# Optimization experiments

Measured on AMD Instinct MI355X. Metric: run time of the kernel, lower is better.

The kernel has to match this reference:

```python
import jax, jax.numpy as jnp
import numpy as np

N_USERS, N_ITEMS, N_TOPICS = 200000, 100000, 100
N_NODES = N_USERS + N_ITEMS + N_TOPICS
N_EDGES = 5000000
DIM = 64
LAYERS = 3
BATCH = 16384


def setup_inputs() -> dict:
    key = jax.random.key(0)
    ks = jax.random.split(key, 8)
    users = jax.random.randint(ks[0], (BATCH,), 0, N_USERS, dtype=jnp.int64 if jax.config.jax_enable_x64 else jnp.int32)
    items = jax.random.randint(ks[1], (BATCH,), 0, N_ITEMS, dtype=jnp.int64 if jax.config.jax_enable_x64 else jnp.int32)
    edge_rows = jax.random.randint(ks[2], (N_EDGES,), 0, N_NODES, dtype=jnp.int32)
    edge_cols = jax.random.randint(ks[3], (N_EDGES,), 0, N_NODES, dtype=jnp.int32)
    # values ~ 1/deg to mimic the symmetric-normalized A_hat of LightGCN
    edge_vals = jax.random.uniform(ks[4], (N_EDGES,), dtype=jnp.float32) / 16.0
    user_emb = 0.1 * jax.random.normal(ks[5], (N_USERS, DIM), dtype=jnp.float32)
    item_emb = 0.1 * jax.random.normal(ks[6], (N_ITEMS, DIM), dtype=jnp.float32)
    topic_emb = 0.1 * jax.random.normal(ks[7], (N_TOPICS, DIM), dtype=jnp.float32)
    return {"users": users, "items": items, "edge_rows": edge_rows,
            "edge_cols": edge_cols, "edge_vals": edge_vals,
            "user_emb": user_emb, "item_emb": item_emb, "topic_emb": topic_emb}


def reference(users, items, edge_rows, edge_cols, edge_vals, user_emb, item_emb, topic_emb):
    n_users = user_emb.shape[0]
    n_nodes = n_users + item_emb.shape[0] + topic_emb.shape[0]
    # E^0 = [users; items; topics]
    h = jnp.concatenate([user_emb, item_emb, topic_emb], axis=0)  # [N, dim]
    acc = h
    for _ in range(LAYERS):
        # sparse A_hat @ h : gather source rows, scale by edge weight, scatter-add to dst
        msgs = edge_vals[:, None] * h[edge_cols]                  # [E, dim]
        h = jax.ops.segment_sum(msgs, edge_rows, num_segments=n_nodes)
        acc = acc + h
    out = acc / (LAYERS + 1)                                      # stack-mean over layers
    u = out[users]                                                # [B, dim]
    it = out[n_users + items]                                     # items offset into node table
    return jnp.sum(u * it, axis=1)                                # [B]
```

## Files before the change

kernel.cpp:

```cpp
#include <hip/hip_runtime.h>
#include <hip/hip_fp16.h>

#define N_USERS  200000
#define N_ITEMS  100000
#define N_TOPICS 100
#define N_NODES  (N_USERS + N_ITEMS + N_TOPICS)
#define DIM      64
#define BSHIFT   10
#define BROWS    (1 << BSHIFT)
#define NBUCKETS ((N_NODES + BROWS - 1) >> BSHIFT)
#define NROWS_PAD (NBUCKETS * BROWS)
#define COLMASK  0x7FFFF
#define NB       512
#define NBSHIFT  9
#define M_TOT    (NBUCKETS * NB)
#define SB       256
#define CH       ((M_TOT + SB - 1) / SB)
#define NCONCAT  (((N_NODES * DIM / 4) + 511) / 512)
#define BUCKET_CAP 24576



__global__ void prep_kernel(const int* __restrict__ rows,
                            int* __restrict__ partial, int n_edges,
                            const float* __restrict__ uemb,
                            const float* __restrict__ iemb,
                            const float* __restrict__ temb,
                            ushort* __restrict__ h0,
                            const int* __restrict__ users,
                            const int* __restrict__ items,
                            float* __restrict__ u_acc,
                            float* __restrict__ it_acc, int B) {
    __shared__ int h[NBUCKETS];
    if (blockIdx.x < NB) {
        for (int i = threadIdx.x; i < NBUCKETS; i += blockDim.x) h[i] = 0;
        __syncthreads();
        int stride = NB * blockDim.x;
        int gid0 = blockIdx.x * blockDim.x + threadIdx.x;
        int n4 = n_edges >> 2;
        const int4* r4 = (const int4*)rows;
        for (int e = gid0; e < n4; e += stride) {
            int4 v = r4[e];
            atomicAdd(&h[((unsigned)v.x) >> BSHIFT], 1);
            atomicAdd(&h[((unsigned)v.y) >> BSHIFT], 1);
            atomicAdd(&h[((unsigned)v.z) >> BSHIFT], 1);
            atomicAdd(&h[((unsigned)v.w) >> BSHIFT], 1);
        }
        for (int e = (n4 << 2) + gid0; e < n_edges; e += stride)
            atomicAdd(&h[((unsigned)rows[e]) >> BSHIFT], 1);
        __syncthreads();
        for (int i = threadIdx.x; i < NBUCKETS; i += blockDim.x)
            partial[blockIdx.x * NBUCKETS + i] = h[i];
    } else if (blockIdx.x < NB + NCONCAT) {
        int g = (blockIdx.x - NB) * blockDim.x + threadIdx.x;
        long base = (long)g * 4;
        if (base >= (long)N_NODES * DIM) return;
        const float* src;
        long off;
        if (base < (long)N_USERS * DIM)                 { src = uemb; off = base; }
        else if (base < (long)(N_USERS + N_ITEMS) * DIM){ src = iemb; off = base - (long)N_USERS * DIM; }
        else                                            { src = temb; off = base - (long)(N_USERS + N_ITEMS) * DIM; }
        float4 v = *(const float4*)(src + off);
        __half2 a = __floats2half2_rn(v.x, v.y);
        __half2 b = __floats2half2_rn(v.z, v.w);
        uint2 o;
        o.x = *(unsigned*)&a;
        o.y = *(unsigned*)&b;
        ((uint2*)h0)[g] = o;
    } else {
        int g = (blockIdx.x - NB - NCONCAT) * blockDim.x + threadIdx.x;
        int b    = g >> 4;
        int lane = g & 15;
        if (b >= B) return;
        int u  = users[b];
        int it = items[b];
        float4 uv = ((const float4*)(uemb + (size_t)u  * DIM))[lane];
        float4 iv = ((const float4*)(iemb + (size_t)it * DIM))[lane];
        ((float4*)(u_acc  + (size_t)b * DIM))[lane] = uv;
        ((float4*)(it_acc + (size_t)b * DIM))[lane] = iv;
    }
}

__device__ __forceinline__ int phys_idx(int L) {
    return (L & (NB - 1)) * NBUCKETS + (L >> NBSHIFT);
}

__global__ void scanB1_kernel(const int* __restrict__ partial,
                              int* __restrict__ psum) {
    __shared__ int s[256];
    int tid = threadIdx.x;
    int c0 = blockIdx.x * CH;
    int c1 = min(M_TOT, c0 + CH);
    int sum = 0;
    for (int L = c0 + tid; L < c1; L += 256) sum += partial[phys_idx(L)];
    s[tid] = sum;
    __syncthreads();
    for (int off = 128; off > 0; off >>= 1) {
        if (tid < off) s[tid] += s[tid + off];
        __syncthreads();
    }
    if (tid == 0) psum[blockIdx.x] = s[0];
}

__global__ void scanB3_kernel(const int* __restrict__ partial,
                              const int* __restrict__ psum,
                              int* __restrict__ offs) {
    __shared__ int s[SB];
    __shared__ int tile[256];
    __shared__ int carry;
    int tid = threadIdx.x;
    s[tid] = (tid < blockIdx.x) ? psum[tid] : 0;
    __syncthreads();
    for (int off = 128; off > 0; off >>= 1) {
        if (tid < off) s[tid] += s[tid + off];
        __syncthreads();
    }
    if (tid == 0) carry = s[0];
    __syncthreads();
    int c0 = blockIdx.x * CH;
    int c1 = min(M_TOT, c0 + CH);
    for (int base = c0; base < c1; base += 256) {
        int L = base + tid;
        int v = (L < c1) ? partial[phys_idx(L)] : 0;
        tile[tid] = v;
        __syncthreads();
        for (int off = 1; off < 256; off <<= 1) {
            int t = (tid >= off) ? tile[tid - off] : 0;
            __syncthreads();
            tile[tid] += t;
            __syncthreads();
        }
        if (L < c1) offs[L] = carry + tile[tid] - v;
        __syncthreads();
        if (tid == 255) carry += tile[255];
        __syncthreads();
    }
}

__global__ void scatter1_kernel(const int* __restrict__ rows,
                                const int* __restrict__ cols,
                                const float* __restrict__ vals,
                                const int* __restrict__ offs,
                                int2* __restrict__ bkt_buf, int n_edges) {
    __shared__ int lpos[NBUCKETS];
    for (int i = threadIdx.x; i < NBUCKETS; i += blockDim.x)
        lpos[i] = offs[i * NB + blockIdx.x];
    __syncthreads();
    int stride = NB * blockDim.x;
    int gid0 = blockIdx.x * blockDim.x + threadIdx.x;
    int n4 = n_edges >> 2;
    const int4*   r4 = (const int4*)rows;
    const int4*   c4 = (const int4*)cols;
    const float4* v4 = (const float4*)vals;
    for (int e = gid0; e < n4; e += stride) {
        int4 r = r4[e];
        int4 c = c4[e];
        float4 v = v4[e];
        #pragma unroll
        for (int j = 0; j < 4; ++j) {
            int rr = (j == 0) ? r.x : (j == 1) ? r.y : (j == 2) ? r.z : r.w;
            int cc = (j == 0) ? c.x : (j == 1) ? c.y : (j == 2) ? c.z : c.w;
            float vv = (j == 0) ? v.x : (j == 1) ? v.y : (j == 2) ? v.z : v.w;
            int b = ((unsigned)rr) >> BSHIFT;
            int pos = atomicAdd(&lpos[b], 1);
            int2 p;
            p.x = cc | ((rr & (BROWS - 1)) << 19);
            p.y = __float_as_int(vv);
            bkt_buf[pos] = p;
        }
    }
    for (int e = (n4 << 2) + gid0; e < n_edges; e += stride) {
        int rr = rows[e];
        int b = ((unsigned)rr) >> BSHIFT;
        int pos = atomicAdd(&lpos[b], 1);
        int2 p;
        p.x = cols[e] | ((rr & (BROWS - 1)) << 19);
        p.y = __float_as_int(vals[e]);
        bkt_buf[pos] = p;
    }
}

__device__ __forceinline__ int pad8(int x) { return (x + 7) & ~7; }

__global__ void scatter2_kernel(const int2* __restrict__ bkt_buf,
                                const int* __restrict__ offs,
                                int2* __restrict__ row_span,
                                int2* __restrict__ csr_cv, int n_edges) {
    __shared__ int lcnt[BROWS];
    __shared__ int lptr[BROWS];
    __shared__ int lfill[BROWS];
    __shared__ int s[512];
    int b = blockIdx.x;
    int t = threadIdx.x;
    int e0 = offs[b * NB];
    int e1 = (b == NBUCKETS - 1) ? n_edges : offs[(b + 1) * NB];
    lcnt[t]  = 0;
    lfill[t] = 0;
    __syncthreads();
    for (int e = e0 + t; e < e1; e += 1024)
        atomicAdd(&lcnt[((unsigned)bkt_buf[e].x) >> 19], 1);
    __syncthreads();
    if (t < 512) s[t] = pad8(lcnt[2 * t]) + pad8(lcnt[2 * t + 1]);
    __syncthreads();
    for (int off = 1; off < 512; off <<= 1) {
        int v = 0;
        if (t < 512 && t >= off) v = s[t - off];
        __syncthreads();
        if (t < 512) s[t] += v;
        __syncthreads();
    }
    if (t < 512) {
        int base = b * BUCKET_CAP + (t ? s[t - 1] : 0);
        int rbase = b << BSHIFT;
        int pe = pad8(lcnt[2 * t]);
        int po = pad8(lcnt[2 * t + 1]);
        int p_even = base;
        int p_odd  = base + pe;
        lptr[2 * t]     = p_even;
        lptr[2 * t + 1] = p_odd;
        int2 sp0; sp0.x = p_even; sp0.y = p_even + pe;
        int2 sp1; sp1.x = p_odd;  sp1.y = p_odd + po;
        row_span[rbase + 2 * t]     = sp0;
        row_span[rbase + 2 * t + 1] = sp1;
    }
    __syncthreads();
    for (int e = e0 + t; e < e1; e += 1024) {
        int2 p = bkt_buf[e];
        int delta = ((unsigned)p.x) >> 19;
        int pos = lptr[delta] + atomicAdd(&lfill[delta], 1);
        int2 cv;
        cv.x = p.x & COLMASK;
        cv.y = p.y;
        csr_cv[pos] = cv;
    }
    __syncthreads();
    {
        int c  = lcnt[t];
        int cp = pad8(c);
        int p  = lptr[t];
        int2 z; z.x = 0; z.y = 0;
        for (int k = c; k < cp; ++k) csr_cv[p + k] = z;
    }
}

__device__ __forceinline__ float4 fma_mix4(const ushort* __restrict__ h,
                                           int row, int l16, float w,
                                           float4 acc) {
    uint2 r = ((const uint2*)(h + (size_t)row * DIM))[l16];
    __half2 h01 = *(__half2*)&r.x;
    __half2 h23 = *(__half2*)&r.y;
    acc.x = __builtin_fmaf(__half2float(__low2half(h01)),  w, acc.x);
    acc.y = __builtin_fmaf(__half2float(__high2half(h01)), w, acc.y);
    acc.z = __builtin_fmaf(__half2float(__low2half(h23)),  w, acc.z);
    acc.w = __builtin_fmaf(__half2float(__high2half(h23)), w, acc.w);
    return acc;
}

__device__ __forceinline__ float4 batch8(const int2* __restrict__ csr_cv,
                                         const ushort* __restrict__ h_src,
                                         int p, int l16, float4 acc) {
    const int4* q = (const int4*)(csr_cv + p);
    int4 a = q[0], b = q[1], c = q[2], d = q[3];
    acc = fma_mix4(h_src, a.x, l16, __int_as_float(a.y), acc);
    acc = fma_mix4(h_src, a.z, l16, __int_as_float(a.w), acc);
    acc = fma_mix4(h_src, b.x, l16, __int_as_float(b.y), acc);
    acc = fma_mix4(h_src, b.z, l16, __int_as_float(b.w), acc);
    acc = fma_mix4(h_src, c.x, l16, __int_as_float(c.y), acc);
    acc = fma_mix4(h_src, c.z, l16, __int_as_float(c.w), acc);
    acc = fma_mix4(h_src, d.x, l16, __int_as_float(d.y), acc);
    acc = fma_mix4(h_src, d.z, l16, __int_as_float(d.w), acc);
    return acc;
}

#define NWAVES ((N_NODES + 3) / 4)

__global__ void spmv_csr_kernel(const int2* __restrict__ row_span,
                                const int2* __restrict__ csr_cv,
                                const ushort* __restrict__ h_src,
                                ushort* __restrict__ h_dst,
                                const int* __restrict__ users,
                                const int* __restrict__ items,
                                float* __restrict__ u_acc,
                                float* __restrict__ it_acc,
                                int B, int first) {
    int wave = (int)(((long)blockIdx.x * blockDim.x + threadIdx.x) >> 6);
    int lane = threadIdx.x & 63;
    int g    = lane >> 4;
    int l16  = lane & 15;
    if (wave < NWAVES) {
        int r    = wave * 4 + g;
        int rc   = min(r, N_NODES - 1);
        int2 sp  = row_span[rc];
        int p0   = sp.x;
        int len  = (r < N_NODES) ? (sp.y - sp.x) : 0;
        int m = max(len, __shfl_xor(len, 16, 64));
        m = max(m, __shfl_xor(m, 32, 64));
        float4 acc = make_float4(0.f, 0.f, 0.f, 0.f);
        for (int off = 0; off < m; off += 8) {
            if (off < len)
                acc = batch8(csr_cv, h_src, p0 + off, l16, acc);
        }
        if (r < N_NODES) {
            __half2 a = __floats2half2_rn(acc.x, acc.y);
            __half2 b = __floats2half2_rn(acc.z, acc.w);
            uint2 o;
            o.x = *(unsigned*)&a;
            o.y = *(unsigned*)&b;
            ((uint2*)(h_dst + (size_t)r * DIM))[l16] = o;
        }
    } else {
        if (first < 0) return;
        int s = (wave - NWAVES) * 4 + g;
        if (s >= 2 * B) return;
        int node = (s < B) ? users[s] : (N_USERS + items[s - B]);
        uint2 hr = ((const uint2*)(h_src + (size_t)node * DIM))[l16];
        float2 a01 = __half22float2(*(__half2*)&hr.x);
        float2 a23 = __half22float2(*(__half2*)&hr.y);
        float* dst = (s < B) ? (u_acc + (size_t)s * DIM)
                             : (it_acc + (size_t)(s - B) * DIM);
        float4* p = (float4*)dst + l16;
        float4 o = *p;
        o.x += a01.x; o.y += a01.y; o.z += a23.x; o.w += a23.y;
        *p = o;
    }
}

__global__ void spmv_batch_dot_kernel(const int2* __restrict__ row_span,
                                      const int2* __restrict__ csr_cv,
                                      const ushort* __restrict__ h_src,
                                      const int* __restrict__ users,
                                      const int* __restrict__ items,
                                      const float* __restrict__ u_acc,
                                      const float* __restrict__ it_acc,
                                      float* __restrict__ out, int B) {
    int wave = (int)(((long)blockIdx.x * blockDim.x + threadIdx.x) >> 6);
    int lane = threadIdx.x & 63;
    int g    = lane >> 4;
    int l16  = lane & 15;
    int b    = wave * 2 + (g >> 1);
    bool ok  = b < B;
    int node = 0;
    if (ok) node = ((g & 1) == 0) ? users[b] : (N_USERS + items[b]);
    float4 acc = make_float4(0.f, 0.f, 0.f, 0.f);
    if (ok) {
        uint2 hr = ((const uint2*)(h_src + (size_t)node * DIM))[l16];
        float2 a01 = __half22float2(*(__half2*)&hr.x);
        float2 a23 = __half22float2(*(__half2*)&hr.y);
        acc = make_float4(a01.x, a01.y, a23.x, a23.y);
    }
    int2 sp  = row_span[ok ? node : 0];
    int p0   = sp.x;
    int len  = ok ? (sp.y - sp.x) : 0;
    int m = max(len, __shfl_xor(len, 16, 64));
    m = max(m, __shfl_xor(m, 32, 64));
    for (int off = 0; off < m; off += 8) {
        if (off < len)
            acc = batch8(csr_cv, h_src, p0 + off, l16, acc);
    }
    if (ok) {
        const float* st = ((g & 1) == 0) ? (u_acc  + (size_t)b * DIM)
                                         : (it_acc + (size_t)b * DIM);
        float4 sv = ((const float4*)st)[l16];
        acc.x += sv.x; acc.y += sv.y; acc.z += sv.z; acc.w += sv.w;
    }
    float px = __shfl_xor(acc.x, 16, 64);
    float py = __shfl_xor(acc.y, 16, 64);
    float pz = __shfl_xor(acc.z, 16, 64);
    float pw = __shfl_xor(acc.w, 16, 64);
    float p = acc.x * px + acc.y * py + acc.z * pz + acc.w * pw;
    p += __shfl_down(p, 8, 16);
    p += __shfl_down(p, 4, 16);
    p += __shfl_down(p, 2, 16);
    p += __shfl_down(p, 1, 16);
    if (ok && (g & 1) == 0 && l16 == 0) out[b] = p * (1.0f / 16.0f);
}

extern "C" void kernel_launch(void* const* d_in, const int* in_sizes, int n_in,
                              void* d_out, int out_size, void* d_ws, size_t ws_size,
                              hipStream_t stream) {
    const int*   users = (const int*)d_in[0];
    const int*   items = (const int*)d_in[1];
    const int*   erows = (const int*)d_in[2];
    const int*   ecols = (const int*)d_in[3];
    const float* evals = (const float*)d_in[4];
    const float* uemb  = (const float*)d_in[5];
    const float* iemb  = (const float*)d_in[6];
    const float* temb  = (const float*)d_in[7];
    float* out = (float*)d_out;

    const int n_edges = in_sizes[2];
    const int B       = in_sizes[0];

    const size_t h2bytes = (((size_t)N_NODES * DIM * 2 + 255) / 256) * 256;
    const size_t abytes  = (size_t)B * DIM * sizeof(float);
    const size_t spbytes = (((size_t)NROWS_PAD * 8 + 255) / 256) * 256;
    const size_t csrbytes= (size_t)NBUCKETS * BUCKET_CAP * 8;
    const size_t bkbytes = (size_t)n_edges * 8;
    const size_t mbytes  = (((size_t)M_TOT * 4 + 255) / 256) * 256;

    char* ws = (char*)d_ws;
    size_t off = 0;
    ushort* hA       = (ushort*)(ws + off); off += h2bytes;
    ushort* hB       = (ushort*)(ws + off); off += h2bytes;
    float*  u_acc    = (float*) (ws + off); off += abytes;
    float*  it_acc   = (float*) (ws + off); off += abytes;
    int2*   row_span = (int2*)  (ws + off); off += spbytes;
    int2*   csr_cv   = (int2*)  (ws + off); off += csrbytes;
    int2*   bkt_buf  = (int2*)  (ws + off); off += bkbytes;
    int*    partial  = (int*)   (ws + off); off += mbytes;
    int*    offs     = (int*)   (ws + off); off += mbytes;
    int*    psum     = (int*)   (ws + off); off += 4096;

    dim3 blk(256);
    dim3 blk512(512);
    dim3 blk1k(1024);

    const int ginit = (B * 16 + 511) / 512;
    prep_kernel<<<NB + NCONCAT + ginit, blk512, 0, stream>>>(
        erows, partial, n_edges, uemb, iemb, temb, hA,
        users, items, u_acc, it_acc, B);
    scanB1_kernel<<<SB, blk, 0, stream>>>(partial, psum);
    scanB3_kernel<<<SB, blk, 0, stream>>>(partial, psum, offs);
    scatter1_kernel<<<NB, blk512, 0, stream>>>(erows, ecols, evals, offs, bkt_buf, n_edges);
    scatter2_kernel<<<NBUCKETS, blk1k, 0, stream>>>(bkt_buf, offs, row_span,
                                                    csr_cv, n_edges);

    const int gwaves  = (2 * B + 3) / 4;
    const int blocks1 = (int)(((long)NWAVES * 64 + 255) / 256);
    const int blocks2 = (int)(((long)(NWAVES + gwaves) * 64 + 255) / 256);
    spmv_csr_kernel<<<blocks1, blk, 0, stream>>>(row_span, csr_cv, hA, hB,
                                                 users, items, u_acc, it_acc, B, -1);
    spmv_csr_kernel<<<blocks2, blk, 0, stream>>>(row_span, csr_cv, hB, hA,
                                                 users, items, u_acc, it_acc, B, 0);
    const int bwaves  = (B + 1) / 2;
    const int bblocks = (int)(((long)bwaves * 64 + 255) / 256);
    spmv_batch_dot_kernel<<<bblocks, blk, 0, stream>>>(row_span, csr_cv, hA,
                                                       users, items, u_acc, it_acc,
                                                       out, B);
}
```

Measured before the change: 502.6 us.

## Fuse the three SpMV layer kernels into one persistent cooperative kernel

Replaces the three separate launches (two SpMV layers and the final SpMV plus batch dot) with a single cooperative persistent kernel. Waves stride over the work, and grid-wide syncs separate the layers. This removes two kernel launch and drain gaps. In exchange, it caps concurrency at the occupancy limit and adds grid.sync overhead. The grid size assumes 256 CUs, which matches MI355X.

```diff
diff --git a/kernel.cpp b/kernel.cpp
--- a/kernel.cpp
+++ b/kernel.cpp
@@ -1,5 +1,8 @@
 #include <hip/hip_runtime.h>
 #include <hip/hip_fp16.h>
+#include <hip/hip_cooperative_groups.h>
+
+namespace cg = cooperative_groups;
 
 #define N_USERS  200000
 #define N_ITEMS  100000
@@ -274,71 +277,67 @@
 
 #define NWAVES ((N_NODES + 3) / 4)
 
-__global__ void spmv_csr_kernel(const int2* __restrict__ row_span,
-                                const int2* __restrict__ csr_cv,
-                                const ushort* __restrict__ h_src,
-                                ushort* __restrict__ h_dst,
-                                const int* __restrict__ users,
-                                const int* __restrict__ items,
-                                float* __restrict__ u_acc,
-                                float* __restrict__ it_acc,
-                                int B, int first) {
-    int wave = (int)(((long)blockIdx.x * blockDim.x + threadIdx.x) >> 6);
-    int lane = threadIdx.x & 63;
-    int g    = lane >> 4;
-    int l16  = lane & 15;
-    if (wave < NWAVES) {
-        int r    = wave * 4 + g;
-        int rc   = min(r, N_NODES - 1);
-        int2 sp  = row_span[rc];
-        int p0   = sp.x;
-        int len  = (r < N_NODES) ? (sp.y - sp.x) : 0;
-        int m = max(len, __shfl_xor(len, 16, 64));
-        m = max(m, __shfl_xor(m, 32, 64));
-        float4 acc = make_float4(0.f, 0.f, 0.f, 0.f);
-        for (int off = 0; off < m; off += 8) {
-            if (off < len)
-                acc = batch8(csr_cv, h_src, p0 + off, l16, acc);
-        }
-        if (r < N_NODES) {
-            __half2 a = __floats2half2_rn(acc.x, acc.y);
-            __half2 b = __floats2half2_rn(acc.z, acc.w);
-            uint2 o;
-            o.x = *(unsigned*)&a;
-            o.y = *(unsigned*)&b;
-            ((uint2*)(h_dst + (size_t)r * DIM))[l16] = o;
-        }
-    } else {
-        if (first < 0) return;
-        int s = (wave - NWAVES) * 4 + g;
-        if (s >= 2 * B) return;
-        int node = (s < B) ? users[s] : (N_USERS + items[s - B]);
-        uint2 hr = ((const uint2*)(h_src + (size_t)node * DIM))[l16];
-        float2 a01 = __half22float2(*(__half2*)&hr.x);
-        float2 a23 = __half22float2(*(__half2*)&hr.y);
-        float* dst = (s < B) ? (u_acc + (size_t)s * DIM)
-                             : (it_acc + (size_t)(s - B) * DIM);
-        float4* p = (float4*)dst + l16;
-        float4 o = *p;
-        o.x += a01.x; o.y += a01.y; o.z += a23.x; o.w += a23.y;
-        *p = o;
-    }
-}
-
-__global__ void spmv_batch_dot_kernel(const int2* __restrict__ row_span,
-                                      const int2* __restrict__ csr_cv,
-                                      const ushort* __restrict__ h_src,
-                                      const int* __restrict__ users,
-                                      const int* __restrict__ items,
-                                      const float* __restrict__ u_acc,
-                                      const float* __restrict__ it_acc,
-                                      float* __restrict__ out, int B) {
-    int wave = (int)(((long)blockIdx.x * blockDim.x + threadIdx.x) >> 6);
-    int lane = threadIdx.x & 63;
-    int g    = lane >> 4;
-    int l16  = lane & 15;
-    int b    = wave * 2 + (g >> 1);
-    bool ok  = b < B;
+__device__ __forceinline__ void spmv_wave(int w,
+                                          const int2* __restrict__ row_span,
+                                          const int2* __restrict__ csr_cv,
+                                          const ushort* __restrict__ h_src,
+                                          ushort* __restrict__ h_dst,
+                                          int g, int l16) {
+    int r    = w * 4 + g;
+    int rc   = min(r, N_NODES - 1);
+    int2 sp  = row_span[rc];
+    int p0   = sp.x;
+    int len  = (r < N_NODES) ? (sp.y - sp.x) : 0;
+    int m = max(len, __shfl_xor(len, 16, 64));
+    m = max(m, __shfl_xor(m, 32, 64));
+    float4 acc = make_float4(0.f, 0.f, 0.f, 0.f);
+    for (int off = 0; off < m; off += 8) {
+        if (off < len)
+            acc = batch8(csr_cv, h_src, p0 + off, l16, acc);
+    }
+    if (r < N_NODES) {
+        __half2 a = __floats2half2_rn(acc.x, acc.y);
+        __half2 b = __floats2half2_rn(acc.z, acc.w);
+        uint2 o;
+        o.x = *(unsigned*)&a;
+        o.y = *(unsigned*)&b;
+        ((uint2*)(h_dst + (size_t)r * DIM))[l16] = o;
+    }
+}
+
+__device__ __forceinline__ void tail_gather(int tw,
+                                            const ushort* __restrict__ h_src,
+                                            const int* __restrict__ users,
+                                            const int* __restrict__ items,
+                                            float* __restrict__ u_acc,
+                                            float* __restrict__ it_acc,
+                                            int B, int g, int l16) {
+    int s = tw * 4 + g;
+    if (s >= 2 * B) return;
+    int node = (s < B) ? users[s] : (N_USERS + items[s - B]);
+    uint2 hr = ((const uint2*)(h_src + (size_t)node * DIM))[l16];
+    float2 a01 = __half22float2(*(__half2*)&hr.x);
+    float2 a23 = __half22float2(*(__half2*)&hr.y);
+    float* dst = (s < B) ? (u_acc + (size_t)s * DIM)
+                         : (it_acc + (size_t)(s - B) * DIM);
+    float4* p = (float4*)dst + l16;
+    float4 o = *p;
+    o.x += a01.x; o.y += a01.y; o.z += a23.x; o.w += a23.y;
+    *p = o;
+}
+
+__device__ __forceinline__ void batch_dot_wave(int w,
+                                               const int2* __restrict__ row_span,
+                                               const int2* __restrict__ csr_cv,
+                                               const ushort* __restrict__ h_src,
+                                               const int* __restrict__ users,
+                                               const int* __restrict__ items,
+                                               const float* __restrict__ u_acc,
+                                               const float* __restrict__ it_acc,
+                                               float* __restrict__ out,
+                                               int B, int g, int l16) {
+    int b   = w * 2 + (g >> 1);
+    bool ok = b < B;
     int node = 0;
     if (ok) node = ((g & 1) == 0) ? users[b] : (N_USERS + items[b]);
     float4 acc = make_float4(0.f, 0.f, 0.f, 0.f);
@@ -373,6 +372,38 @@
     p += __shfl_down(p, 2, 16);
     p += __shfl_down(p, 1, 16);
     if (ok && (g & 1) == 0 && l16 == 0) out[b] = p * (1.0f / 16.0f);
+}
+
+__global__ __launch_bounds__(256, 8)
+void gcn_layers_kernel(const int2* __restrict__ row_span,
+                       const int2* __restrict__ csr_cv,
+                       ushort* __restrict__ hA,
+                       ushort* __restrict__ hB,
+                       const int* __restrict__ users,
+                       const int* __restrict__ items,
+                       float* __restrict__ u_acc,
+                       float* __restrict__ it_acc,
+                       float* __restrict__ out, int B) {
+    cg::grid_group grid = cg::this_grid();
+    int lane = threadIdx.x & 63;
+    int g    = lane >> 4;
+    int l16  = lane & 15;
+    int gwid = (int)(((long)blockIdx.x * blockDim.x + threadIdx.x) >> 6);
+    int gstr = (gridDim.x * blockDim.x) >> 6;
+    int gw   = (2 * B + 3) / 4;
+
+    for (int w = gwid; w < NWAVES; w += gstr)
+        spmv_wave(w, row_span, csr_cv, hA, hB, g, l16);
+    grid.sync();
+    for (int w = gwid; w < NWAVES + gw; w += gstr) {
+        if (w < NWAVES) spmv_wave(w, row_span, csr_cv, hB, hA, g, l16);
+        else tail_gather(w - NWAVES, hB, users, items, u_acc, it_acc, B, g, l16);
+    }
+    grid.sync();
+    int bw = (B + 1) / 2;
+    for (int w = gwid; w < bw; w += gstr)
+        batch_dot_wave(w, row_span, csr_cv, hA, users, items,
+                       u_acc, it_acc, out, B, g, l16);
 }
 
 extern "C" void kernel_launch(void* const* d_in, const int* in_sizes, int n_in,
@@ -425,16 +456,15 @@
     scatter2_kernel<<<NBUCKETS, blk1k, 0, stream>>>(bkt_buf, offs, row_span,
                                                     csr_cv, n_edges);
 
-    const int gwaves  = (2 * B + 3) / 4;
-    const int blocks1 = (int)(((long)NWAVES * 64 + 255) / 256);
-    const int blocks2 = (int)(((long)(NWAVES + gwaves) * 64 + 255) / 256);
-    spmv_csr_kernel<<<blocks1, blk, 0, stream>>>(row_span, csr_cv, hA, hB,
-                                                 users, items, u_acc, it_acc, B, -1);
-    spmv_csr_kernel<<<blocks2, blk, 0, stream>>>(row_span, csr_cv, hB, hA,
-                                                 users, items, u_acc, it_acc, B, 0);
-    const int bwaves  = (B + 1) / 2;
-    const int bblocks = (int)(((long)bwaves * 64 + 255) / 256);
-    spmv_batch_dot_kernel<<<bblocks, blk, 0, stream>>>(row_span, csr_cv, hA,
-                                                       users, items, u_acc, it_acc,
-                                                       out, B);
-}
+    int nblk = 0;
+    hipOccupancyMaxActiveBlocksPerMultiprocessor(&nblk, gcn_layers_kernel, 256, 0);
+    if (nblk < 1) nblk = 1;
+    if (nblk > 8) nblk = 8;
+    int coop_grid = nblk * 256;
+    int Bv = B;
+    void* kargs[] = {(void*)&row_span, (void*)&csr_cv, (void*)&hA, (void*)&hB,
+                     (void*)&users, (void*)&items, (void*)&u_acc, (void*)&it_acc,
+                     (void*)&out, (void*)&Bv};
+    hipLaunchCooperativeKernel((void*)gcn_layers_kernel, dim3(coop_grid),
+                               dim3(256), kargs, 0, stream);
+}
```

Result: slower. 808.4 us (+60.9%).
